# Performance work log

Hardware: AMD Instinct MI355X
Metric: run time of the kernel (lower is better)

Reference implementation:

```python
import jax, jax.numpy as jnp
import numpy as np

N = 100000      # nodes
E = 3200000     # directed edges (before self loops)
F_IN = 512      # input node features
HID = 16        # hidden dim (hardcoded in module)
C = 32          # num_classes
NEG_SLOPE = 0.2 # PyG GATConv default


def setup_inputs() -> dict:
    key = jax.random.key(0)
    ks = jax.random.split(key, 10)
    x = jax.random.normal(ks[0], (N, F_IN), dtype=jnp.float32)
    edge_index = jax.random.randint(ks[1], (2, E), 0, N, dtype=jnp.int64)
    s1 = 1.0 / np.sqrt(F_IN)
    s2 = 1.0 / np.sqrt(HID)
    return {
        "x": x,
        "edge_index": edge_index,
        "W1": jax.random.normal(ks[2], (F_IN, HID), dtype=jnp.float32) * s1,
        "att_src1": jax.random.normal(ks[3], (HID,), dtype=jnp.float32) * s2,
        "att_dst1": jax.random.normal(ks[4], (HID,), dtype=jnp.float32) * s2,
        "b1": jnp.zeros((HID,), dtype=jnp.float32),
        "W2": jax.random.normal(ks[5], (HID, C), dtype=jnp.float32) * s2,
        "att_src2": jax.random.normal(ks[6], (C,), dtype=jnp.float32) / np.sqrt(C),
        "att_dst2": jax.random.normal(ks[7], (C,), dtype=jnp.float32) / np.sqrt(C),
        "b2": jnp.zeros((C,), dtype=jnp.float32),
    }


def gat_conv(h_in, src, dst, W, att_src, att_dst, b, n):
    # h: [n, d_out] transformed node features (lin has no bias in PyG GATConv)
    h = h_in @ W
    a_s = h @ att_src        # [n] per-node source score
    a_d = h @ att_dst        # [n] per-node dest score
    e = jax.nn.leaky_relu(a_s[src] + a_d[dst], NEG_SLOPE)  # [n_edges]
    # segment softmax over edges grouped by destination node
    m = jax.ops.segment_max(e, dst, num_segments=n)
    ex = jnp.exp(e - m[dst])
    denom = jax.ops.segment_sum(ex, dst, num_segments=n)
    alpha = ex / denom[dst]
    out = jax.ops.segment_sum(h[src] * alpha[:, None], dst, num_segments=n)
    return out + b


def reference(x, edge_index, W1, att_src1, att_dst1, b1, W2, att_src2, att_dst2, b2):
    n = x.shape[0]
    loops = jnp.arange(n, dtype=edge_index.dtype)  # add_self_loops=True
    src = jnp.concatenate([edge_index[0], loops])
    dst = jnp.concatenate([edge_index[1], loops])
    h = gat_conv(x, src, dst, W1, att_src1, att_dst1, b1, n)
    h = jax.nn.relu(h)
    # dropout is identity in eval mode
    out = gat_conv(h, src, dst, W2, att_src2, att_dst2, b2, n)
    return jax.nn.log_softmax(out, axis=1)
```

## Files before the change

kernel.cpp:

```cpp
#include <hip/hip_runtime.h>
#include <math.h>

#define N_NODES 100000
#define N_EDGES 3200000
#define N_TOT   (N_EDGES + N_NODES)
#define F_IN    512
#define HID     16
#define NCLS    32
#define NEG_SLOPE 0.2f

#define BSH   7
#define NBKT  ((N_NODES + 127) / 128)
#define SRC_MASK 0x1FFFF

#define G_GROUPS 512
#define EPG (N_EDGES / G_GROUPS)

__global__ __launch_bounds__(64) void k_detect(const int* __restrict__ ei,
                                               int* __restrict__ flag) {
  int v = ei[2 * threadIdx.x + 1];
  unsigned long long m = __ballot(v != 0);
  if (threadIdx.x == 0) *flag = (m == 0ull) ? 1 : 0;
}

__global__ __launch_bounds__(256) void k_hist(const int* __restrict__ ei,
                                              const int* __restrict__ flag,
                                              int* __restrict__ H) {
  __shared__ int h[NBKT];
  for (int i = threadIdx.x; i < NBKT; i += 256) h[i] = 0;
  __syncthreads();
  int fl = *flag;
  int g = blockIdx.x;
  int e0 = g * EPG, e1 = e0 + EPG;
  for (int e = e0 + threadIdx.x; e < e1; e += 256) {
    int d = fl ? ei[2 * (N_EDGES + e)] : ei[N_EDGES + e];
    d = min(max(d, 0), N_NODES - 1);
    atomicAdd(&h[d >> BSH], 1);
  }
  __syncthreads();
  int* Hrow = H + (size_t)g * NBKT;
  for (int i = threadIdx.x; i < NBKT; i += 256) Hrow[i] = h[i];
}

__global__ __launch_bounds__(G_GROUPS) void k_colscan(int* __restrict__ H,
                                                      int* __restrict__ tot) {
  __shared__ int s[G_GROUPS];
  int b = blockIdx.x, t = threadIdx.x;
  int v = H[(size_t)t * NBKT + b];
  s[t] = v;
  __syncthreads();
  for (int off = 1; off < G_GROUPS; off <<= 1) {
    int a = (t >= off) ? s[t - off] : 0;
    __syncthreads();
    s[t] += a;
    __syncthreads();
  }
  H[(size_t)t * NBKT + b] = s[t] - v;
  if (t == G_GROUPS - 1) tot[b] = s[t];
}

__global__ __launch_bounds__(256) void k_bscan(const int* __restrict__ tot,
                                               int* __restrict__ bbase,
                                               int* __restrict__ cbase,
                                               int* __restrict__ offs) {
  __shared__ int s1[256], s2[256];
  int t = threadIdx.x;
  int c[4], vn[4];
  int sum1 = 0, sum2 = 0;
#pragma unroll
  for (int j = 0; j < 4; ++j) {
    int idx = t * 4 + j;
    int cc = 0, vv = 0;
    if (idx < NBKT) {
      cc = tot[idx];
      int lo = idx << BSH;
      vv = min(128, N_NODES - lo);
    }
    c[j] = cc; vn[j] = vv;
    sum1 += cc; sum2 += cc + vv;
  }
  int o1 = sum1, o2 = sum2;
  s1[t] = sum1; s2[t] = sum2;
  __syncthreads();
  for (int off = 1; off < 256; off <<= 1) {
    int a = 0, b = 0;
    if (t >= off) { a = s1[t - off]; b = s2[t - off]; }
    __syncthreads();
    s1[t] += a; s2[t] += b;
    __syncthreads();
  }
  int r1 = s1[t] - o1;
  int r2 = s2[t] - o2;
#pragma unroll
  for (int j = 0; j < 4; ++j) {
    int idx = t * 4 + j;
    if (idx < NBKT) {
      bbase[idx] = r1; cbase[idx] = r2;
      r1 += c[j];
      r2 += c[j] + vn[j];
    }
  }
  if (t == 0) offs[N_NODES] = N_TOT;
}

__global__ __launch_bounds__(256) void k_scatter(const int* __restrict__ ei,
                                                 const int* __restrict__ flag,
                                                 const int* __restrict__ H,
                                                 const int* __restrict__ bbase,
                                                 int* __restrict__ binned) {
  __shared__ int cur[NBKT];
  int g = blockIdx.x, t = threadIdx.x;
  const int* Hrow = H + (size_t)g * NBKT;
  for (int i = t; i < NBKT; i += 256) cur[i] = bbase[i] + Hrow[i];
  __syncthreads();
  int fl = *flag;
  int e0 = g * EPG, e1 = e0 + EPG;
  for (int e = e0 + t; e < e1; e += 256) {
    int s, d;
    if (fl) { s = ei[2 * e]; d = ei[2 * (N_EDGES + e)]; }
    else    { s = ei[e];     d = ei[N_EDGES + e]; }
    s = min(max(s, 0), N_NODES - 1);
    d = min(max(d, 0), N_NODES - 1);
    int p = atomicAdd(&cur[d >> BSH], 1);
    p = min(max(p, 0), N_EDGES - 1);
    binned[p] = ((d & 127) << 17) | s;
  }
}

__global__ __launch_bounds__(256) void k_bucket(const int* __restrict__ tot,
                                                const int* __restrict__ bbase,
                                                const int* __restrict__ cbase,
                                                const int* __restrict__ binned,
                                                int* __restrict__ offs,
                                                int* __restrict__ srcS) {
  __shared__ int cnt[128], cur[128], sc[128];
  __shared__ int hdr[3];
  int b = blockIdx.x, t = threadIdx.x;
  if (t == 0) {
    hdr[0] = min(max(tot[b], 0), N_EDGES);
    hdr[1] = min(max(bbase[b], 0), N_EDGES - 1);
    hdr[2] = min(max(cbase[b], 0), N_TOT - 1);
  }
  if (t < 128) cnt[t] = 0;
  __syncthreads();
  int nb = hdr[0], base = hdr[1], cb = hdr[2];

  for (int i = t; i < nb; i += 256) {
    int pk = binned[min(base + i, N_EDGES - 1)];
    atomicAdd(&cnt[(pk >> 17) & 127], 1);
  }
  __syncthreads();

  int node = (b << BSH) + t;
  int myv = 0;
  if (t < 128) myv = (node < N_NODES) ? cnt[t] + 1 : 0;
  if (t < 128) sc[t] = myv;
  __syncthreads();
  for (int off = 1; off < 128; off <<= 1) {
    int v = 0;
    if (t < 128 && t >= off) v = sc[t - off];
    __syncthreads();
    if (t < 128) sc[t] += v;
    __syncthreads();
  }
  if (t < 128 && node < N_NODES) {
    int lofs = sc[t] - myv;
    int o = min(cb + lofs, N_TOT - 1);
    offs[node] = o;
    srcS[o] = node;
    cur[t] = lofs + 1;
  }
  __syncthreads();

  for (int i = t; i < nb; i += 256) {
    int pk = binned[min(base + i, N_EDGES - 1)];
    int p = atomicAdd(&cur[(pk >> 17) & 127], 1);
    srcS[min(cb + p, N_TOT - 1)] = pk & SRC_MASK;
  }
}

__global__ __launch_bounds__(64) void k_prep(const float* __restrict__ W2,
                                             const float* __restrict__ as2w,
                                             const float* __restrict__ ad2w,
                                             float* __restrict__ ws2,
                                             float* __restrict__ wd2) {
  int t = threadIdx.x;
  if (t < HID) {
    float s = 0.f, d = 0.f;
    for (int c = 0; c < NCLS; ++c) {
      float wv = W2[t * NCLS + c];
      s += wv * as2w[c];
      d += wv * ad2w[c];
    }
    ws2[t] = s;
    wd2[t] = d;
  }
}

__global__ __launch_bounds__(512) void k_gemm1(const float* __restrict__ x,
                                               const float* __restrict__ W,
                                               const float* __restrict__ atts,
                                               const float* __restrict__ attd,
                                               float* __restrict__ h,
                                               float* __restrict__ as_,
                                               float* __restrict__ ad_) {
  __shared__ float xs[2][128][36];
  float* pacc = &xs[0][0][0];
  int t = threadIdx.x;
  int wid = t >> 6;
  int lane = t & 63;
  int rhalf = wid & 1;
  int kq = __builtin_amdgcn_readfirstlane(wid >> 1);
  int row = rhalf * 64 + lane;
  int r0 = blockIdx.x * 128;

  int sr = t >> 3;
  int sk4 = t & 7;
  int sr2 = (t + 512) >> 3;
  int sk42 = (t + 512) & 7;
  int gr1 = min(r0 + sr, N_NODES - 1);
  int gr2 = min(r0 + sr2, N_NODES - 1);

  float acc[HID];
#pragma unroll
  for (int f = 0; f < HID; ++f) acc[f] = 0.f;

  float4 ra, rb;
  ra = *(const float4*)(x + (size_t)gr1 * F_IN + sk4 * 4);
  rb = *(const float4*)(x + (size_t)gr2 * F_IN + sk42 * 4);
  *(float4*)(&xs[0][sr][sk4 * 4]) = ra;
  *(float4*)(&xs[0][sr2][sk42 * 4]) = rb;
  __syncthreads();

  for (int c = 0; c < F_IN / 32; ++c) {
    int buf = c & 1;
    if (c + 1 < F_IN / 32) {
      ra = *(const float4*)(x + (size_t)gr1 * F_IN + (c + 1) * 32 + sk4 * 4);
      rb = *(const float4*)(x + (size_t)gr2 * F_IN + (c + 1) * 32 + sk42 * 4);
    }
    const float* Wc = W + (c * 32 + kq * 8) * HID;
    float4 xa = *(const float4*)(&xs[buf][row][kq * 8 + 0]);
    float4 xb = *(const float4*)(&xs[buf][row][kq * 8 + 4]);
#pragma unroll
    for (int f = 0; f < HID; ++f)
      acc[f] += xa.x * Wc[0 * HID + f] + xa.y * Wc[1 * HID + f] +
                xa.z * Wc[2 * HID + f] + xa.w * Wc[3 * HID + f];
#pragma unroll
    for (int f = 0; f < HID; ++f)
      acc[f] += xb.x * Wc[4 * HID + f] + xb.y * Wc[5 * HID + f] +
                xb.z * Wc[6 * HID + f] + xb.w * Wc[7 * HID + f];
    if (c + 1 < F_IN / 32) {
      *(float4*)(&xs[buf ^ 1][sr][sk4 * 4]) = ra;
      *(float4*)(&xs[buf ^ 1][sr2][sk42 * 4]) = rb;
    }
    __syncthreads();
  }

#pragma unroll
  for (int f = 0; f < HID; ++f) pacc[(kq * 128 + row) * 17 + f] = acc[f];
  __syncthreads();

  int rr = t >> 2, g = t & 3;
  float4 s;
  s.x = pacc[(0 * 128 + rr) * 17 + g * 4 + 0] + pacc[(1 * 128 + rr) * 17 + g * 4 + 0] +
        pacc[(2 * 128 + rr) * 17 + g * 4 + 0] + pacc[(3 * 128 + rr) * 17 + g * 4 + 0];
  s.y = pacc[(0 * 128 + rr) * 17 + g * 4 + 1] + pacc[(1 * 128 + rr) * 17 + g * 4 + 1] +
        pacc[(2 * 128 + rr) * 17 + g * 4 + 1] + pacc[(3 * 128 + rr) * 17 + g * 4 + 1];
  s.z = pacc[(0 * 128 + rr) * 17 + g * 4 + 2] + pacc[(1 * 128 + rr) * 17 + g * 4 + 2] +
        pacc[(2 * 128 + rr) * 17 + g * 4 + 2] + pacc[(3 * 128 + rr) * 17 + g * 4 + 2];
  s.w = pacc[(0 * 128 + rr) * 17 + g * 4 + 3] + pacc[(1 * 128 + rr) * 17 + g * 4 + 3] +
        pacc[(2 * 128 + rr) * 17 + g * 4 + 3] + pacc[(3 * 128 + rr) * 17 + g * 4 + 3];
  int orow = r0 + rr;
  if (orow < N_NODES) ((float4*)(h + (size_t)orow * HID))[g] = s;

  float4 av = ((const float4*)atts)[g];
  float4 dv = ((const float4*)attd)[g];
  float pas = s.x * av.x + s.y * av.y + s.z * av.z + s.w * av.w;
  float pad = s.x * dv.x + s.y * dv.y + s.z * dv.z + s.w * dv.w;
  pas += __shfl_xor(pas, 1); pas += __shfl_xor(pas, 2);
  pad += __shfl_xor(pad, 1); pad += __shfl_xor(pad, 2);
  if (g == 0 && orow < N_NODES) { as_[orow] = pas; ad_[orow] = pad; }
}

template <bool LAYER1>
__global__ __launch_bounds__(256) void k_agg(const int* __restrict__ offs,
                                             const int* __restrict__ srcS,
                                             const float* __restrict__ as_,
                                             const float* __restrict__ ad_,
                                             const float* __restrict__ h,
                                             const float* __restrict__ b1,
                                             const float* __restrict__ ws2,
                                             const float* __restrict__ wd2,
                                             float* __restrict__ outv,
                                             float* __restrict__ as2,
                                             float* __restrict__ ad2) {
  int node = blockIdx.x * 4 + (threadIdx.x >> 6);
  if (node >= N_NODES) return;
  int lane = threadIdx.x & 63;
  int esub = lane >> 2;
  int f4 = lane & 3;
  int beg = offs[node];
  int end = offs[node + 1];
  beg = min(max(beg, 0), N_TOT);
  end = min(max(end, beg), N_TOT);
  float ad = ad_[node];

  float s_lane = 0.f;
  float4 acc = make_float4(0.f, 0.f, 0.f, 0.f);
  for (int i0 = beg; i0 < end; i0 += 64) {
    int nb = min(64, end - i0);
    int sn = 0;
    float p = 0.f;
    if (lane < nb) {
      sn = min(max(srcS[i0 + lane], 0), N_NODES - 1);
      float e = as_[sn] + ad;
      e = e > 0.f ? e : NEG_SLOPE * e;
      p = __expf(e);
    }
    s_lane += p;
    int steps = (nb + 15) >> 4;
    for (int t = 0; t < steps; ++t) {
      int j = esub + 16 * t;
      int jj = min(j, nb - 1);
      float pj = __shfl(p, jj);
      int snj = __shfl(sn, jj);
      if (j < nb) {
        float4 v = ((const float4*)(h + (size_t)snj * HID))[f4];
        acc.x += pj * v.x;
        acc.y += pj * v.y;
        acc.z += pj * v.z;
        acc.w += pj * v.w;
      }
    }
  }
#pragma unroll
  for (int off = 1; off < 64; off <<= 1) s_lane += __shfl_xor(s_lane, off);
#pragma unroll
  for (int off = 4; off < 64; off <<= 1) {
    acc.x += __shfl_xor(acc.x, off);
    acc.y += __shfl_xor(acc.y, off);
    acc.z += __shfl_xor(acc.z, off);
    acc.w += __shfl_xor(acc.w, off);
  }
  float inv_s = 1.f / s_lane;

  if (LAYER1) {
    float4 bv = ((const float4*)b1)[f4];
    float4 val;
    val.x = fmaxf(acc.x * inv_s + bv.x, 0.f);
    val.y = fmaxf(acc.y * inv_s + bv.y, 0.f);
    val.z = fmaxf(acc.z * inv_s + bv.z, 0.f);
    val.w = fmaxf(acc.w * inv_s + bv.w, 0.f);
    if (lane < 4) ((float4*)(outv + (size_t)node * HID))[lane] = val;
    float4 w_s = ((const float4*)ws2)[f4];
    float4 w_d = ((const float4*)wd2)[f4];
    float rs = val.x * w_s.x + val.y * w_s.y + val.z * w_s.z + val.w * w_s.w;
    float rd = val.x * w_d.x + val.y * w_d.y + val.z * w_d.z + val.w * w_d.w;
    rs += __shfl_xor(rs, 1); rs += __shfl_xor(rs, 2);
    rd += __shfl_xor(rd, 1); rd += __shfl_xor(rd, 2);
    if (lane == 0) { as2[node] = rs; ad2[node] = rd; }
  } else {
    float4 val;
    val.x = acc.x * inv_s;
    val.y = acc.y * inv_s;
    val.z = acc.z * inv_s;
    val.w = acc.w * inv_s;
    if (lane < 4) ((float4*)(outv + (size_t)node * HID))[lane] = val;
  }
}

__global__ __launch_bounds__(256) void k_out(const float* __restrict__ agg2,
                                             const float* __restrict__ W2,
                                             const float* __restrict__ b2,
                                             float* __restrict__ out) {
  int row = blockIdx.x * 256 + threadIdx.x;
  if (row >= N_NODES) return;
  float hv[HID];
  const float4* hp = (const float4*)(agg2 + (size_t)row * HID);
#pragma unroll
  for (int j = 0; j < 4; ++j) {
    float4 v = hp[j];
    hv[4 * j] = v.x; hv[4 * j + 1] = v.y; hv[4 * j + 2] = v.z; hv[4 * j + 3] = v.w;
  }
  float acc[NCLS];
#pragma unroll
  for (int c = 0; c < NCLS; ++c) acc[c] = b2[c];
#pragma unroll
  for (int k = 0; k < HID; ++k) {
    float xv = hv[k];
    const float* Wr = W2 + k * NCLS;
#pragma unroll
    for (int c = 0; c < NCLS; ++c) acc[c] += xv * Wr[c];
  }
  float mx = -1e30f;
#pragma unroll
  for (int c = 0; c < NCLS; ++c) mx = fmaxf(mx, acc[c]);
  float se = 0.f;
#pragma unroll
  for (int c = 0; c < NCLS; ++c) se += __expf(acc[c] - mx);
  float lse = mx + __logf(se);
  float4* op = (float4*)(out + (size_t)row * NCLS);
#pragma unroll
  for (int j = 0; j < 8; ++j)
    op[j] = make_float4(acc[4 * j] - lse, acc[4 * j + 1] - lse,
                        acc[4 * j + 2] - lse, acc[4 * j + 3] - lse);
}

extern "C" void kernel_launch(void* const* d_in, const int* in_sizes, int n_in,
                              void* d_out, int out_size, void* d_ws, size_t ws_size,
                              hipStream_t stream) {
  const float* x    = (const float*)d_in[0];
  const int*   ei   = (const int*)d_in[1];
  const float* W1   = (const float*)d_in[2];
  const float* as1w = (const float*)d_in[3];
  const float* ad1w = (const float*)d_in[4];
  const float* b1   = (const float*)d_in[5];
  const float* W2   = (const float*)d_in[6];
  const float* as2w = (const float*)d_in[7];
  const float* ad2w = (const float*)d_in[8];
  const float* b2   = (const float*)d_in[9];
  float* out = (float*)d_out;

  char* w = (char*)d_ws;
  size_t off = 0;
  auto alloc = [&](size_t bytes) -> char* {
    char* p = w + off;
    off += (bytes + 511) & ~(size_t)511;
    return p;
  };
  int*   flag  = (int*)alloc(4);
  int*   tot   = (int*)alloc((size_t)NBKT * 4);
  int*   bbase = (int*)alloc((size_t)NBKT * 4);
  int*   cbase = (int*)alloc((size_t)NBKT * 4);
  int*   offs  = (int*)alloc((size_t)(N_NODES + 1) * 4);
  int*   srcS  = (int*)alloc((size_t)N_TOT * 4);
  float* ws2   = (float*)alloc((size_t)HID * 4);
  float* wd2   = (float*)alloc((size_t)HID * 4);

  size_t region_begin = off;
  int* binned = (int*)alloc((size_t)N_EDGES * 4);
  int* H      = (int*)alloc((size_t)G_GROUPS * NBKT * 4);
  off = region_begin;
  float* h1   = (float*)alloc((size_t)N_NODES * HID * 4);
  float* as1  = (float*)alloc((size_t)N_NODES * 4);
  float* ad1  = (float*)alloc((size_t)N_NODES * 4);
  float* hr   = (float*)alloc((size_t)N_NODES * HID * 4);
  float* agg2 = (float*)alloc((size_t)N_NODES * HID * 4);
  float* as2  = (float*)alloc((size_t)N_NODES * 4);
  float* ad2  = (float*)alloc((size_t)N_NODES * 4);

  k_detect<<<1, 64, 0, stream>>>(ei, flag);
  k_hist<<<G_GROUPS, 256, 0, stream>>>(ei, flag, H);
  k_colscan<<<NBKT, G_GROUPS, 0, stream>>>(H, tot);
  k_bscan<<<1, 256, 0, stream>>>(tot, bbase, cbase, offs);
  k_scatter<<<G_GROUPS, 256, 0, stream>>>(ei, flag, H, bbase, binned);
  k_bucket<<<NBKT, 256, 0, stream>>>(tot, bbase, cbase, binned, offs, srcS);
  k_gemm1<<<(N_NODES + 127) / 128, 512, 0, stream>>>(x, W1, as1w, ad1w, h1, as1, ad1);
  k_prep<<<1, 64, 0, stream>>>(W2, as2w, ad2w, ws2, wd2);
  k_agg<true><<<(N_NODES + 3) / 4, 256, 0, stream>>>(offs, srcS, as1, ad1, h1,
                                                     b1, ws2, wd2, hr, as2, ad2);
  k_agg<false><<<(N_NODES + 3) / 4, 256, 0, stream>>>(offs, srcS, as2, ad2, hr,
                                                      nullptr, nullptr, nullptr,
                                                      agg2, nullptr, nullptr);
  k_out<<<(N_NODES + 255) / 256, 256, 0, stream>>>(agg2, W2, b2, out);
}
```

Baseline: 276.5 us.

## Merge GEMM1, histogram and prep into one launch; fuse output head into layer-2 aggregation

```diff
diff --git a/kernel.cpp b/kernel.cpp
--- a/kernel.cpp
+++ b/kernel.cpp
@@ -15,6 +15,7 @@
 
 #define G_GROUPS 512
 #define EPG (N_EDGES / G_GROUPS)
+#define NGEMM ((N_NODES + 127) / 128)
 
 __global__ __launch_bounds__(64) void k_detect(const int* __restrict__ ei,
                                                int* __restrict__ flag) {
@@ -23,23 +24,131 @@
   if (threadIdx.x == 0) *flag = (m == 0ull) ? 1 : 0;
 }
 
-__global__ __launch_bounds__(256) void k_hist(const int* __restrict__ ei,
-                                              const int* __restrict__ flag,
-                                              int* __restrict__ H) {
-  __shared__ int h[NBKT];
-  for (int i = threadIdx.x; i < NBKT; i += 256) h[i] = 0;
-  __syncthreads();
-  int fl = *flag;
-  int g = blockIdx.x;
-  int e0 = g * EPG, e1 = e0 + EPG;
-  for (int e = e0 + threadIdx.x; e < e1; e += 256) {
-    int d = fl ? ei[2 * (N_EDGES + e)] : ei[N_EDGES + e];
-    d = min(max(d, 0), N_NODES - 1);
-    atomicAdd(&h[d >> BSH], 1);
-  }
-  __syncthreads();
-  int* Hrow = H + (size_t)g * NBKT;
-  for (int i = threadIdx.x; i < NBKT; i += 256) Hrow[i] = h[i];
+__global__ __launch_bounds__(512) void k_g1h(const float* __restrict__ x,
+                                             const float* __restrict__ W,
+                                             const float* __restrict__ atts,
+                                             const float* __restrict__ attd,
+                                             const int* __restrict__ ei,
+                                             const int* __restrict__ flag,
+                                             int* __restrict__ H,
+                                             const float* __restrict__ W2,
+                                             const float* __restrict__ as2w,
+                                             const float* __restrict__ ad2w,
+                                             float* __restrict__ ws2,
+                                             float* __restrict__ wd2,
+                                             float* __restrict__ h,
+                                             float* __restrict__ as_,
+                                             float* __restrict__ ad_) {
+  __shared__ float smem[2 * 128 * 36];
+  int bid = blockIdx.x;
+  int t = threadIdx.x;
+
+  if (bid >= NGEMM) {
+    if (bid < NGEMM + G_GROUPS) {
+      int* hh = (int*)smem;
+      for (int i = t; i < NBKT; i += 512) hh[i] = 0;
+      __syncthreads();
+      int fl = *flag;
+      int g = bid - NGEMM;
+      int e0 = g * EPG, e1 = e0 + EPG;
+      for (int e = e0 + t; e < e1; e += 512) {
+        int d = fl ? ei[2 * (N_EDGES + e)] : ei[N_EDGES + e];
+        d = min(max(d, 0), N_NODES - 1);
+        atomicAdd(&hh[d >> BSH], 1);
+      }
+      __syncthreads();
+      int* Hrow = H + (size_t)g * NBKT;
+      for (int i = t; i < NBKT; i += 512) Hrow[i] = hh[i];
+    } else {
+      if (t < HID) {
+        float s = 0.f, d = 0.f;
+        for (int c = 0; c < NCLS; ++c) {
+          float wv = W2[t * NCLS + c];
+          s += wv * as2w[c];
+          d += wv * ad2w[c];
+        }
+        ws2[t] = s;
+        wd2[t] = d;
+      }
+    }
+    return;
+  }
+
+  float (*xs)[128][36] = (float (*)[128][36])smem;
+  float* pacc = smem;
+  int wid = t >> 6;
+  int lane = t & 63;
+  int rhalf = wid & 1;
+  int kq = __builtin_amdgcn_readfirstlane(wid >> 1);
+  int row = rhalf * 64 + lane;
+  int r0 = bid * 128;
+
+  int sr = t >> 3;
+  int sk4 = t & 7;
+  int sr2 = (t + 512) >> 3;
+  int sk42 = (t + 512) & 7;
+  int gr1 = min(r0 + sr, N_NODES - 1);
+  int gr2 = min(r0 + sr2, N_NODES - 1);
+
+  float acc[HID];
+#pragma unroll
+  for (int f = 0; f < HID; ++f) acc[f] = 0.f;
+
+  float4 ra, rb;
+  ra = *(const float4*)(x + (size_t)gr1 * F_IN + sk4 * 4);
+  rb = *(const float4*)(x + (size_t)gr2 * F_IN + sk42 * 4);
+  *(float4*)(&xs[0][sr][sk4 * 4]) = ra;
+  *(float4*)(&xs[0][sr2][sk42 * 4]) = rb;
+  __syncthreads();
+
+  for (int c = 0; c < F_IN / 32; ++c) {
+    int buf = c & 1;
+    if (c + 1 < F_IN / 32) {
+      ra = *(const float4*)(x + (size_t)gr1 * F_IN + (c + 1) * 32 + sk4 * 4);
+      rb = *(const float4*)(x + (size_t)gr2 * F_IN + (c + 1) * 32 + sk42 * 4);
+    }
+    const float* Wc = W + (c * 32 + kq * 8) * HID;
+    float4 xa = *(const float4*)(&xs[buf][row][kq * 8 + 0]);
+    float4 xb = *(const float4*)(&xs[buf][row][kq * 8 + 4]);
+#pragma unroll
+    for (int f = 0; f < HID; ++f)
+      acc[f] += xa.x * Wc[0 * HID + f] + xa.y * Wc[1 * HID + f] +
+                xa.z * Wc[2 * HID + f] + xa.w * Wc[3 * HID + f];
+#pragma unroll
+    for (int f = 0; f < HID; ++f)
+      acc[f] += xb.x * Wc[4 * HID + f] + xb.y * Wc[5 * HID + f] +
+                xb.z * Wc[6 * HID + f] + xb.w * Wc[7 * HID + f];
+    if (c + 1 < F_IN / 32) {
+      *(float4*)(&xs[buf ^ 1][sr][sk4 * 4]) = ra;
+      *(float4*)(&xs[buf ^ 1][sr2][sk42 * 4]) = rb;
+    }
+    __syncthreads();
+  }
+
+#pragma unroll
+  for (int f = 0; f < HID; ++f) pacc[(kq * 128 + row) * 17 + f] = acc[f];
+  __syncthreads();
+
+  int rr = t >> 2, g = t & 3;
+  float4 s;
+  s.x = pacc[(0 * 128 + rr) * 17 + g * 4 + 0] + pacc[(1 * 128 + rr) * 17 + g * 4 + 0] +
+        pacc[(2 * 128 + rr) * 17 + g * 4 + 0] + pacc[(3 * 128 + rr) * 17 + g * 4 + 0];
+  s.y = pacc[(0 * 128 + rr) * 17 + g * 4 + 1] + pacc[(1 * 128 + rr) * 17 + g * 4 + 1] +
+        pacc[(2 * 128 + rr) * 17 + g * 4 + 1] + pacc[(3 * 128 + rr) * 17 + g * 4 + 1];
+  s.z = pacc[(0 * 128 + rr) * 17 + g * 4 + 2] + pacc[(1 * 128 + rr) * 17 + g * 4 + 2] +
+        pacc[(2 * 128 + rr) * 17 + g * 4 + 2] + pacc[(3 * 128 + rr) * 17 + g * 4 + 2];
+  s.w = pacc[(0 * 128 + rr) * 17 + g * 4 + 3] + pacc[(1 * 128 + rr) * 17 + g * 4 + 3] +
+        pacc[(2 * 128 + rr) * 17 + g * 4 + 3] + pacc[(3 * 128 + rr) * 17 + g * 4 + 3];
+  int orow = r0 + rr;
+  if (orow < N_NODES) ((float4*)(h + (size_t)orow * HID))[g] = s;
+
+  float4 av = ((const float4*)atts)[g];
+  float4 dv = ((const float4*)attd)[g];
+  float pas = s.x * av.x + s.y * av.y + s.z * av.z + s.w * av.w;
+  float pad = s.x * dv.x + s.y * dv.y + s.z * dv.z + s.w * dv.w;
+  pas += __shfl_xor(pas, 1); pas += __shfl_xor(pas, 2);
+  pad += __shfl_xor(pad, 1); pad += __shfl_xor(pad, 2);
+  if (g == 0 && orow < N_NODES) { as_[orow] = pas; ad_[orow] = pad; }
 }
 
 __global__ __launch_bounds__(G_GROUPS) void k_colscan(int* __restrict__ H,
@@ -179,109 +288,6 @@
   }
 }
 
-__global__ __launch_bounds__(64) void k_prep(const float* __restrict__ W2,
-                                             const float* __restrict__ as2w,
-                                             const float* __restrict__ ad2w,
-                                             float* __restrict__ ws2,
-                                             float* __restrict__ wd2) {
-  int t = threadIdx.x;
-  if (t < HID) {
-    float s = 0.f, d = 0.f;
-    for (int c = 0; c < NCLS; ++c) {
-      float wv = W2[t * NCLS + c];
-      s += wv * as2w[c];
-      d += wv * ad2w[c];
-    }
-    ws2[t] = s;
-    wd2[t] = d;
-  }
-}
-
-__global__ __launch_bounds__(512) void k_gemm1(const float* __restrict__ x,
-                                               const float* __restrict__ W,
-                                               const float* __restrict__ atts,
-                                               const float* __restrict__ attd,
-                                               float* __restrict__ h,
-                                               float* __restrict__ as_,
-                                               float* __restrict__ ad_) {
-  __shared__ float xs[2][128][36];
-  float* pacc = &xs[0][0][0];
-  int t = threadIdx.x;
-  int wid = t >> 6;
-  int lane = t & 63;
-  int rhalf = wid & 1;
-  int kq = __builtin_amdgcn_readfirstlane(wid >> 1);
-  int row = rhalf * 64 + lane;
-  int r0 = blockIdx.x * 128;
-
-  int sr = t >> 3;
-  int sk4 = t & 7;
-  int sr2 = (t + 512) >> 3;
-  int sk42 = (t + 512) & 7;
-  int gr1 = min(r0 + sr, N_NODES - 1);
-  int gr2 = min(r0 + sr2, N_NODES - 1);
-
-  float acc[HID];
-#pragma unroll
-  for (int f = 0; f < HID; ++f) acc[f] = 0.f;
-
-  float4 ra, rb;
-  ra = *(const float4*)(x + (size_t)gr1 * F_IN + sk4 * 4);
-  rb = *(const float4*)(x + (size_t)gr2 * F_IN + sk42 * 4);
-  *(float4*)(&xs[0][sr][sk4 * 4]) = ra;
-  *(float4*)(&xs[0][sr2][sk42 * 4]) = rb;
-  __syncthreads();
-
-  for (int c = 0; c < F_IN / 32; ++c) {
-    int buf = c & 1;
-    if (c + 1 < F_IN / 32) {
-      ra = *(const float4*)(x + (size_t)gr1 * F_IN + (c + 1) * 32 + sk4 * 4);
-      rb = *(const float4*)(x + (size_t)gr2 * F_IN + (c + 1) * 32 + sk42 * 4);
-    }
-    const float* Wc = W + (c * 32 + kq * 8) * HID;
-    float4 xa = *(const float4*)(&xs[buf][row][kq * 8 + 0]);
-    float4 xb = *(const float4*)(&xs[buf][row][kq * 8 + 4]);
-#pragma unroll
-    for (int f = 0; f < HID; ++f)
-      acc[f] += xa.x * Wc[0 * HID + f] + xa.y * Wc[1 * HID + f] +
-                xa.z * Wc[2 * HID + f] + xa.w * Wc[3 * HID + f];
-#pragma unroll
-    for (int f = 0; f < HID; ++f)
-      acc[f] += xb.x * Wc[4 * HID + f] + xb.y * Wc[5 * HID + f] +
-                xb.z * Wc[6 * HID + f] + xb.w * Wc[7 * HID + f];
-    if (c + 1 < F_IN / 32) {
-      *(float4*)(&xs[buf ^ 1][sr][sk4 * 4]) = ra;
-      *(float4*)(&xs[buf ^ 1][sr2][sk42 * 4]) = rb;
-    }
-    __syncthreads();
-  }
-
-#pragma unroll
-  for (int f = 0; f < HID; ++f) pacc[(kq * 128 + row) * 17 + f] = acc[f];
-  __syncthreads();
-
-  int rr = t >> 2, g = t & 3;
-  float4 s;
-  s.x = pacc[(0 * 128 + rr) * 17 + g * 4 + 0] + pacc[(1 * 128 + rr) * 17 + g * 4 + 0] +
-        pacc[(2 * 128 + rr) * 17 + g * 4 + 0] + pacc[(3 * 128 + rr) * 17 + g * 4 + 0];
-  s.y = pacc[(0 * 128 + rr) * 17 + g * 4 + 1] + pacc[(1 * 128 + rr) * 17 + g * 4 + 1] +
-        pacc[(2 * 128 + rr) * 17 + g * 4 + 1] + pacc[(3 * 128 + rr) * 17 + g * 4 + 1];
-  s.z = pacc[(0 * 128 + rr) * 17 + g * 4 + 2] + pacc[(1 * 128 + rr) * 17 + g * 4 + 2] +
-        pacc[(2 * 128 + rr) * 17 + g * 4 + 2] + pacc[(3 * 128 + rr) * 17 + g * 4 + 2];
-  s.w = pacc[(0 * 128 + rr) * 17 + g * 4 + 3] + pacc[(1 * 128 + rr) * 17 + g * 4 + 3] +
-        pacc[(2 * 128 + rr) * 17 + g * 4 + 3] + pacc[(3 * 128 + rr) * 17 + g * 4 + 3];
-  int orow = r0 + rr;
-  if (orow < N_NODES) ((float4*)(h + (size_t)orow * HID))[g] = s;
-
-  float4 av = ((const float4*)atts)[g];
-  float4 dv = ((const float4*)attd)[g];
-  float pas = s.x * av.x + s.y * av.y + s.z * av.z + s.w * av.w;
-  float pad = s.x * dv.x + s.y * dv.y + s.z * dv.z + s.w * dv.w;
-  pas += __shfl_xor(pas, 1); pas += __shfl_xor(pas, 2);
-  pad += __shfl_xor(pad, 1); pad += __shfl_xor(pad, 2);
-  if (g == 0 && orow < N_NODES) { as_[orow] = pas; ad_[orow] = pad; }
-}
-
 template <bool LAYER1>
 __global__ __launch_bounds__(256) void k_agg(const int* __restrict__ offs,
                                              const int* __restrict__ srcS,
@@ -291,6 +297,8 @@
                                              const float* __restrict__ b1,
                                              const float* __restrict__ ws2,
                                              const float* __restrict__ wd2,
+                                             const float* __restrict__ W2,
+                                             const float* __restrict__ b2,
                                              float* __restrict__ outv,
                                              float* __restrict__ as2,
                                              float* __restrict__ ad2) {
@@ -360,50 +368,28 @@
     rd += __shfl_xor(rd, 1); rd += __shfl_xor(rd, 2);
     if (lane == 0) { as2[node] = rs; ad2[node] = rd; }
   } else {
-    float4 val;
-    val.x = acc.x * inv_s;
-    val.y = acc.y * inv_s;
-    val.z = acc.z * inv_s;
-    val.w = acc.w * inv_s;
-    if (lane < 4) ((float4*)(outv + (size_t)node * HID))[lane] = val;
-  }
-}
-
-__global__ __launch_bounds__(256) void k_out(const float* __restrict__ agg2,
-                                             const float* __restrict__ W2,
-                                             const float* __restrict__ b2,
-                                             float* __restrict__ out) {
-  int row = blockIdx.x * 256 + threadIdx.x;
-  if (row >= N_NODES) return;
-  float hv[HID];
-  const float4* hp = (const float4*)(agg2 + (size_t)row * HID);
-#pragma unroll
-  for (int j = 0; j < 4; ++j) {
-    float4 v = hp[j];
-    hv[4 * j] = v.x; hv[4 * j + 1] = v.y; hv[4 * j + 2] = v.z; hv[4 * j + 3] = v.w;
-  }
-  float acc[NCLS];
-#pragma unroll
-  for (int c = 0; c < NCLS; ++c) acc[c] = b2[c];
-#pragma unroll
-  for (int k = 0; k < HID; ++k) {
-    float xv = hv[k];
-    const float* Wr = W2 + k * NCLS;
-#pragma unroll
-    for (int c = 0; c < NCLS; ++c) acc[c] += xv * Wr[c];
-  }
-  float mx = -1e30f;
-#pragma unroll
-  for (int c = 0; c < NCLS; ++c) mx = fmaxf(mx, acc[c]);
-  float se = 0.f;
-#pragma unroll
-  for (int c = 0; c < NCLS; ++c) se += __expf(acc[c] - mx);
-  float lse = mx + __logf(se);
-  float4* op = (float4*)(out + (size_t)row * NCLS);
-#pragma unroll
-  for (int j = 0; j < 8; ++j)
-    op[j] = make_float4(acc[4 * j] - lse, acc[4 * j + 1] - lse,
-                        acc[4 * j + 2] - lse, acc[4 * j + 3] - lse);
+    float hv[HID];
+#pragma unroll
+    for (int j = 0; j < 4; ++j) {
+      int srcl = (lane & ~3) | j;
+      hv[4 * j + 0] = __shfl(acc.x, srcl) * inv_s;
+      hv[4 * j + 1] = __shfl(acc.y, srcl) * inv_s;
+      hv[4 * j + 2] = __shfl(acc.z, srcl) * inv_s;
+      hv[4 * j + 3] = __shfl(acc.w, srcl) * inv_s;
+    }
+    int c = lane & 31;
+    float logit = b2[c];
+#pragma unroll
+    for (int k = 0; k < HID; ++k) logit += hv[k] * W2[k * NCLS + c];
+    float mx = logit;
+#pragma unroll
+    for (int off = 1; off < 32; off <<= 1) mx = fmaxf(mx, __shfl_xor(mx, off));
+    float ex = __expf(logit - mx);
+    float se = ex;
+#pragma unroll
+    for (int off = 1; off < 32; off <<= 1) se += __shfl_xor(se, off);
+    if (lane < 32) outv[(size_t)node * NCLS + c] = logit - mx - __logf(se);
+  }
 }
 
 extern "C" void kernel_launch(void* const* d_in, const int* in_sizes, int n_in,
@@ -436,31 +422,30 @@
   int*   srcS  = (int*)alloc((size_t)N_TOT * 4);
   float* ws2   = (float*)alloc((size_t)HID * 4);
   float* wd2   = (float*)alloc((size_t)HID * 4);
+  int*   H     = (int*)alloc((size_t)G_GROUPS * NBKT * 4);
+  float* h1    = (float*)alloc((size_t)N_NODES * HID * 4);
+  float* as1   = (float*)alloc((size_t)N_NODES * 4);
+  float* ad1   = (float*)alloc((size_t)N_NODES * 4);
 
   size_t region_begin = off;
   int* binned = (int*)alloc((size_t)N_EDGES * 4);
-  int* H      = (int*)alloc((size_t)G_GROUPS * NBKT * 4);
   off = region_begin;
-  float* h1   = (float*)alloc((size_t)N_NODES * HID * 4);
-  float* as1  = (float*)alloc((size_t)N_NODES * 4);
-  float* ad1  = (float*)alloc((size_t)N_NODES * 4);
   float* hr   = (float*)alloc((size_t)N_NODES * HID * 4);
-  float* agg2 = (float*)alloc((size_t)N_NODES * HID * 4);
   float* as2  = (float*)alloc((size_t)N_NODES * 4);
   float* ad2  = (float*)alloc((size_t)N_NODES * 4);
 
   k_detect<<<1, 64, 0, stream>>>(ei, flag);
-  k_hist<<<G_GROUPS, 256, 0, stream>>>(ei, flag, H);
+  k_g1h<<<NGEMM + G_GROUPS + 1, 512, 0, stream>>>(x, W1, as1w, ad1w, ei, flag, H,
+                                                  W2, as2w, ad2w, ws2, wd2,
+                                                  h1, as1, ad1);
   k_colscan<<<NBKT, G_GROUPS, 0, stream>>>(H, tot);
   k_bscan<<<1, 256, 0, stream>>>(tot, bbase, cbase, offs);
   k_scatter<<<G_GROUPS, 256, 0, stream>>>(ei, flag, H, bbase, binned);
   k_bucket<<<NBKT, 256, 0, stream>>>(tot, bbase, cbase, binned, offs, srcS);
-  k_gemm1<<<(N_NODES + 127) / 128, 512, 0, stream>>>(x, W1, as1w, ad1w, h1, as1, ad1);
-  k_prep<<<1, 64, 0, stream>>>(W2, as2w, ad2w, ws2, wd2);
   k_agg<true><<<(N_NODES + 3) / 4, 256, 0, stream>>>(offs, srcS, as1, ad1, h1,
-                                                     b1, ws2, wd2, hr, as2, ad2);
+                                                     b1, ws2, wd2, nullptr, nullptr,
+                                                     hr, as2, ad2);
   k_agg<false><<<(N_NODES + 3) / 4, 256, 0, stream>>>(offs, srcS, as2, ad2, hr,
                                                       nullptr, nullptr, nullptr,
-                                                      agg2, nullptr, nullptr);
-  k_out<<<(N_NODES + 255) / 256, 256, 0, stream>>>(agg2, W2, b2, out);
-}
+                                                      W2, b2, out, nullptr, nullptr);
+}
```

New measurement: 267.3 us. 1.03x faster.
